# Optimization experiments

Hardware: AMD Instinct MI355X
Metric: run time of the kernel (lower is better)

## Reference

```python
import jax, jax.numpy as jnp
import numpy as np

B, N, C, H = 16, 1024, 768, 12
HD = C // H  # head_dim = 64


def setup_inputs() -> dict:
    key = jax.random.key(0)
    ks = jax.random.split(key, 3)
    scale = 1.0 / np.sqrt(C)
    x = jax.random.normal(ks[0], (B, N, C), dtype=jnp.float32)
    Wqkv = jax.random.normal(ks[1], (C, 3 * C), dtype=jnp.float32) * scale
    bqkv = jnp.zeros((3 * C,), dtype=jnp.float32)
    Wout = jax.random.normal(ks[2], (C, C), dtype=jnp.float32) * scale
    bout = jnp.zeros((C,), dtype=jnp.float32)
    return {"x": x, "Wqkv": Wqkv, "bqkv": bqkv, "Wout": Wout, "bout": bout}


def reference(x, Wqkv, bqkv, Wout, bout):
    # QKV projection: [B,N,3C] -> [B,N,3,H,HD]
    qkv = (x @ Wqkv + bqkv).reshape(B, N, 3, H, HD)
    q = qkv[:, :, 0].transpose(0, 2, 1, 3)  # [B,H,N,HD]
    k = qkv[:, :, 1].transpose(0, 2, 1, 3)
    v = qkv[:, :, 2].transpose(0, 2, 1, 3)
    # Patch attention (the only path that reaches the output: the source's
    # cross-image attention result is overwritten before out_proj, so it is
    # dead code). Dropout is identity in eval mode.
    scores = jnp.einsum("bhqd,bhkd->bhqk", q, k) / np.sqrt(HD).astype(np.float32)
    attn = jax.nn.softmax(scores, axis=-1)
    out = jnp.einsum("bhqk,bhkd->bhqd", attn, v)  # [B,H,N,HD]
    out = out.transpose(0, 2, 1, 3).reshape(B, N, C)
    return out @ Wout + bout
```

## Files before the change

kernel.cpp:

```cpp
#include <hip/hip_runtime.h>
#include <hip/hip_bf16.h>

#define B_   16
#define N_   1024
#define C_   768
#define H_   12
#define HD_  64
#define M_   16384
#define N1_  2304
#define NEG_BIG (-1e30f)
#define LOG2E 1.4426950408889634f

typedef __attribute__((ext_vector_type(8))) _Float16 f16x8;
typedef __attribute__((ext_vector_type(4))) float f32x4;
typedef __attribute__((ext_vector_type(16))) float f32x16;

__device__ __forceinline__ unsigned short f2h(float f) {
  _Float16 h = (_Float16)f;
  union { _Float16 h; unsigned short u; } c; c.h = h; return c.u;
}
__device__ __forceinline__ unsigned int cvtpk_f16(float a, float b) {
  unsigned int r;
  asm("v_cvt_pkrtz_f16_f32 %0, %1, %2" : "=v"(r) : "v"(a), "v"(b));
  return r;
}
__device__ __forceinline__ float exp2_asm(float x) {
  float r;
  asm("v_exp_f32 %0, %1" : "=v"(r) : "v"(x));
  return r;
}

__device__ __forceinline__ void gload_lds16(const void* g, void* l) {
  __builtin_amdgcn_global_load_lds(
      (const __attribute__((address_space(1))) void*)g,
      (__attribute__((address_space(3))) void*)l, 16, 0, 0);
}


typedef __attribute__((ext_vector_type(8))) short u16x8;

__global__ __launch_bounds__(256) void k_cvt_x(const float* __restrict__ x,
                                               unsigned short* __restrict__ xh) {
  long i = ((long)blockIdx.x * 256 + threadIdx.x) * 8;
  float4 a = *(const float4*)(x + i);
  float4 b = *(const float4*)(x + i + 4);
  u16x8 v;
  v[0] = (short)f2h(a.x); v[1] = (short)f2h(a.y);
  v[2] = (short)f2h(a.z); v[3] = (short)f2h(a.w);
  v[4] = (short)f2h(b.x); v[5] = (short)f2h(b.y);
  v[6] = (short)f2h(b.z); v[7] = (short)f2h(b.w);
  *(u16x8*)(xh + i) = v;
}

__global__ __launch_bounds__(256) void k_prep_wqkvT(const float* __restrict__ W,
                                                    unsigned short* __restrict__ Wt) {
  int tid = blockIdx.x * 256 + threadIdx.x;
  int n  = tid % N1_;
  int kc = tid / N1_;
  u16x8 v;
#pragma unroll
  for (int j = 0; j < 8; ++j)
    v[j] = (short)f2h(W[(long)(kc * 8 + j) * N1_ + n]);
  *(u16x8*)(Wt + (long)n * C_ + kc * 8) = v;
}

__global__ __launch_bounds__(256) void k_prep_wout(const float* __restrict__ W,
                                                   unsigned short* __restrict__ Wt) {
  int tid = blockIdx.x * 256 + threadIdx.x;
  int n  = tid % C_;
  int kc = tid / C_;
  u16x8 v;
#pragma unroll
  for (int j = 0; j < 8; ++j)
    v[j] = (short)f2h(W[(long)(kc * 8 + j) * C_ + n]);
  *(u16x8*)(Wt + (long)n * C_ + kc * 8) = v;
}

__global__ __launch_bounds__(256) void k_transposeV2(const unsigned short* __restrict__ qkvb,
                                                     unsigned short* __restrict__ Vt) {
  __shared__ unsigned char lt[16384];
  int wid = (blockIdx.x & 7) * 192 + (blockIdx.x >> 3);
  int bh = wid >> 3, nb = wid & 7;
  int b = bh / H_, h = bh % H_;
  long tok0 = (long)b * N_ + nb * 128;
  int t = threadIdx.x;
  int d0 = (t & 7) * 8;
#pragma unroll
  for (int it = 0; it < 4; ++it) {
    int nl = it * 32 + (t >> 3);
    u16x8 v = *(const u16x8*)(qkvb + (tok0 + nl) * N1_ + 1536 + h * HD_ + d0);
#pragma unroll
    for (int j = 0; j < 8; ++j) {
      int d = d0 + j;
      *(unsigned short*)(lt + d * 256 + ((nl * 2) ^ (((d >> 3) & 7) << 4))) =
          (unsigned short)v[j];
    }
  }
  __syncthreads();
  int l = t & 63, wv = t >> 6;
  int p = l & 1;
  int dbase = ((l >> 1) & 7) * 8 + (l >> 4) * 2;
#pragma unroll
  for (int rr = 0; rr < 4; ++rr) {
    int d = dbase + (rr & 1);
    int n0 = wv * 32 + (rr >> 1) * 16 + p * 8;
    u16x8 v = *(const u16x8*)(lt + d * 256 + ((n0 * 2) ^ (((d >> 3) & 7) << 4)));
    *(u16x8*)(Vt + ((long)bh * HD_ + d) * N_ + nb * 128 + n0) = v;
  }
}

template <int STAGE>
__global__ __launch_bounds__(512, 2)
void gemm256(const unsigned short* __restrict__ A,
             const unsigned short* __restrict__ Bt,
             const float* __restrict__ bias,
             void* __restrict__ out, int Kdim, int Ndim) {
  extern __shared__ unsigned char lds[];
  const int t = threadIdx.x;
  const int l = t & 63, w = t >> 6;
  const int g = l >> 4, lr = l & 15;
  const int wm = w >> 2, wn = w & 3;
  const int NB = Ndim >> 8;
  const int wgid = (blockIdx.x & 7) * (gridDim.x >> 3) + (blockIdx.x >> 3);
  const int mb = wgid / NB, nb = wgid % NB;
  const long m0 = (long)mb << 8, n0 = (long)nb << 8;
  const int T = Kdim >> 6;

  f32x4 acc[8][4];
  const f32x4 zz = {0.f, 0.f, 0.f, 0.f};
#pragma unroll
  for (int i = 0; i < 8; ++i)
#pragma unroll
    for (int j = 0; j < 4; ++j) acc[i][j] = zz;

  const long K2 = (long)Kdim * 2;
  const char* Ab = (const char*)A;
  const char* Bb = (const char*)Bt;
  const int sxcol = ((t & 7) * 16) ^ (((t >> 3) & 7) << 4);
  const int srowk = t >> 3;
  const int wvbase = w * 1024;

#define STAGE_A2(tile, i0)                                                   \
  {                                                                          \
    unsigned char* bufb_ = lds + ((tile) & 1) * 65536;                       \
    const char* As_ = Ab + (m0 + srowk) * K2 + (long)(tile) * 128 + sxcol;   \
    gload_lds16(As_ + (long)((i0) * 64) * K2,                                \
                (void*)(bufb_ + (i0) * 8192 + wvbase));                      \
    gload_lds16(As_ + (long)(((i0) + 1) * 64) * K2,                          \
                (void*)(bufb_ + ((i0) + 1) * 8192 + wvbase));                \
  }
#define STAGE_B2(tile, i0)                                                   \
  {                                                                          \
    unsigned char* bufb_ = lds + ((tile) & 1) * 65536 + 32768;               \
    const char* Bs_ = Bb + (n0 + srowk) * K2 + (long)(tile) * 128 + sxcol;   \
    gload_lds16(Bs_ + (long)((i0) * 64) * K2,                                \
                (void*)(bufb_ + (i0) * 8192 + wvbase));                      \
    gload_lds16(Bs_ + (long)(((i0) + 1) * 64) * K2,                          \
                (void*)(bufb_ + ((i0) + 1) * 8192 + wvbase));                \
  }

#define READ_A(ks, base)                                                     \
  _Pragma("unroll")                                                          \
  for (int mf = 0; mf < 8; ++mf) {                                           \
    int row = wm * 128 + mf * 16 + lr;                                       \
    af[mf] = *(const f16x8*)((base) + row * 128 +                            \
                             (((ks) * 64 + g * 16) ^ ((row & 7) << 4)));     \
  }
#define READ_B(ks, nh, base)                                                 \
  _Pragma("unroll")                                                          \
  for (int nf = 0; nf < 2; ++nf) {                                           \
    int row = wn * 64 + (nh) * 32 + nf * 16 + lr;                            \
    bfr[nf] = *(const f16x8*)((base) + 32768 + row * 128 +                   \
                              (((ks) * 64 + g * 16) ^ ((row & 7) << 4)));    \
  }
#define MFMA16(nh)                                                           \
  _Pragma("unroll")                                                          \
  for (int mf = 0; mf < 8; ++mf) {                                           \
    acc[mf][(nh) * 2 + 0] = __builtin_amdgcn_mfma_f32_16x16x32_f16(          \
        af[mf], bfr[0], acc[mf][(nh) * 2 + 0], 0, 0, 0);                     \
    acc[mf][(nh) * 2 + 1] = __builtin_amdgcn_mfma_f32_16x16x32_f16(          \
        af[mf], bfr[1], acc[mf][(nh) * 2 + 1], 0, 0, 0);                     \
  }
#define BAR()  __builtin_amdgcn_s_barrier(); asm volatile("" ::: "memory")

  STAGE_A2(0, 0); STAGE_A2(0, 2); STAGE_B2(0, 0); STAGE_B2(0, 2);
  STAGE_A2(1, 0); STAGE_A2(1, 2); STAGE_B2(1, 0); STAGE_B2(1, 2);
  asm volatile("s_waitcnt vmcnt(8)" ::: "memory");
  BAR();

  for (int tt = 0; tt < T; ++tt) {
    unsigned char* base = lds + (tt & 1) * 65536;
    f16x8 af[8], bfr[2];
    READ_A(0, base);
    READ_B(0, 0, base);
    if (tt >= 1 && tt + 1 < T) STAGE_B2(tt + 1, 0);
    BAR();
    __builtin_amdgcn_s_setprio(1);
    MFMA16(0);
    __builtin_amdgcn_s_setprio(0);
    BAR();
    READ_B(0, 1, base);
    if (tt >= 1 && tt + 1 < T) STAGE_B2(tt + 1, 2);
    BAR();
    __builtin_amdgcn_s_setprio(1);
    MFMA16(1);
    __builtin_amdgcn_s_setprio(0);
    BAR();
    READ_A(1, base);
    READ_B(1, 0, base);
    if (tt >= 1 && tt + 1 < T) STAGE_A2(tt + 1, 2);
    BAR();
    __builtin_amdgcn_s_setprio(1);
    MFMA16(0);
    __builtin_amdgcn_s_setprio(0);
    BAR();
    READ_B(1, 1, base);
    if (tt + 2 < T) STAGE_A2(tt + 2, 0);
    BAR();
    __builtin_amdgcn_s_setprio(1);
    MFMA16(1);
    __builtin_amdgcn_s_setprio(0);
    if (tt + 1 < T) {
      if (tt + 2 < T) { asm volatile("s_waitcnt vmcnt(2)" ::: "memory"); }
      else            { asm volatile("s_waitcnt vmcnt(0)" ::: "memory"); }
    }
    BAR();
  }
#undef STAGE_A2
#undef STAGE_B2
#undef READ_A
#undef READ_B
#undef MFMA16

  if (STAGE == 1) {
    float sc = (n0 < 768) ? 0.125f * LOG2E : 1.0f;
    unsigned short* cl = (unsigned short*)lds;
#pragma unroll
    for (int j = 0; j < 4; ++j) {
      int col = wn * 64 + (j >> 1) * 32 + (j & 1) * 16 + lr;
      float bv = bias[(int)n0 + col];
#pragma unroll
      for (int mf = 0; mf < 8; ++mf)
#pragma unroll
        for (int r = 0; r < 4; ++r) {
          int row = wm * 128 + mf * 16 + g * 4 + r;
          cl[row * 256 + col] = f2h((acc[mf][j][r] + bv) * sc);
        }
    }
    __syncthreads();
    unsigned short* o = (unsigned short*)out;
#pragma unroll
    for (int it = 0; it < 16; ++it) {
      int idx = it * 4096 + t * 8;
      int row = idx >> 8;
      int col = idx & 255;
      *(u16x8*)(o + (m0 + row) * N1_ + n0 + col) = *(const u16x8*)(cl + idx);
    }
  } else {
    float* o = (float*)out;
#pragma unroll
    for (int j = 0; j < 4; ++j) {
      int col = (int)n0 + wn * 64 + (j >> 1) * 32 + (j & 1) * 16 + lr;
      float bv = bias[col];
#pragma unroll
      for (int mf = 0; mf < 8; ++mf)
#pragma unroll
        for (int r = 0; r < 4; ++r) {
          long rowm = m0 + wm * 128 + mf * 16 + g * 4 + r;
          o[rowm * C_ + col] = acc[mf][j][r] + bv;
        }
    }
  }
#undef BAR
}

__global__ __launch_bounds__(256, 3)
void attn_fused(const unsigned short* __restrict__ qkvb,
                const unsigned short* __restrict__ Vt,
                unsigned short* __restrict__ Ofp) {
  __shared__ unsigned char lds[32768];
  const int t = threadIdx.x, l = t & 63, w = t >> 6;
  const int q32 = l & 31;
  const int hi = l >> 5;
  const int hi16 = hi * 16;
  const int wid = (blockIdx.x & 7) * 192 + (blockIdx.x >> 3);
  const int bh = wid >> 3, qb = wid & 7;
  const int b = bh / H_, h = bh % H_;
  const long tok0 = (long)b * N_;
  const int q0 = qb * 128 + w * 32;
  const long mytok = tok0 + q0 + q32;

  f16x8 qa[4];
#pragma unroll
  for (int cs = 0; cs < 4; ++cs)
    qa[cs] = *(const f16x8*)(qkvb + mytok * N1_ + h * HD_ + cs * 16 + hi * 8);

  const f32x16 zz16 = {0.f};
  f32x16 o0 = zz16, o1 = zz16;
  float mrun = NEG_BIG, lrun = 0.f;

  const int row0 = q32, row1 = 32 + q32;
  const int swz0 = (q32 & 7) << 4;

  const int sxs = ((t & 7) * 16) ^ (((t >> 3) & 7) << 4);
  const int wbase = (t & 192) * 16;
  const char* Vg = (const char*)(Vt + (long)bh * HD_ * N_);
  const char* Kg = (const char*)qkvb + ((tok0)*N1_ + C_ + h * HD_) * 2;

#define STAGE_KV(kv0, buf)                                                  \
  {                                                                         \
    _Pragma("unroll")                                                       \
    for (int i = 0; i < 2; ++i) {                                           \
      int row = i * 32 + (t >> 3);                                          \
      gload_lds16(Kg + ((long)(kv0 + row) * N1_) * 2 + sxs,                 \
                  (void*)((buf) + i * 4096 + wbase));                       \
    }                                                                       \
    _Pragma("unroll")                                                       \
    for (int i = 0; i < 2; ++i) {                                           \
      int row = i * 32 + (t >> 3);                                          \
      gload_lds16(Vg + ((long)row * N_ + (kv0)) * 2 + sxs,                  \
                  (void*)((buf) + 8192 + i * 4096 + wbase));                \
    }                                                                       \
  }

  STAGE_KV(0, lds);

#pragma unroll 2
  for (int tt = 0; tt < 16; ++tt) {
    unsigned char* curb = lds + (tt & 1) * 16384;
    unsigned char* nxtb = lds + ((tt & 1) ^ 1) * 16384;
    if (tt < 15) {
      STAGE_KV((tt + 1) * 64, nxtb);
      asm volatile("s_waitcnt vmcnt(4)" ::: "memory");
    } else {
      asm volatile("s_waitcnt vmcnt(0)" ::: "memory");
    }
    __builtin_amdgcn_s_barrier();
    __builtin_amdgcn_sched_barrier(0);

    f32x16 sa0 = zz16, sa1 = zz16;
#pragma unroll
    for (int cs = 0; cs < 4; ++cs) {
      f16x8 kf0 = *(const f16x8*)(curb + row0 * 128 + ((cs * 32 + hi16) ^ swz0));
      f16x8 kf1 = *(const f16x8*)(curb + row1 * 128 + ((cs * 32 + hi16) ^ swz0));
      sa0 = __builtin_amdgcn_mfma_f32_32x32x16_f16(kf0, qa[cs], sa0, 0, 0, 0);
      sa1 = __builtin_amdgcn_mfma_f32_32x32x16_f16(kf1, qa[cs], sa1, 0, 0, 0);
    }

    float tm[16];
#pragma unroll
    for (int i = 0; i < 16; ++i) tm[i] = fmaxf(sa0[i], sa1[i]);
#pragma unroll
    for (int s = 8; s >= 1; s >>= 1)
#pragma unroll
      for (int i = 0; i < s; ++i) tm[i] = fmaxf(tm[i], tm[i + s]);
    float mx = tm[0];
    mx = fmaxf(mx, __shfl_xor(mx, 32));
    if (!__all(mx <= mrun + 8.f)) {
      float mn = fmaxf(mrun, mx);
      float al = exp2_asm(mrun - mn);
      mrun = mn;
      lrun *= al;
      o0 *= al;
      o1 *= al;
    }
    float p0a[16], p1a[16];
#pragma unroll
    for (int i = 0; i < 16; ++i) p0a[i] = exp2_asm(sa0[i] - mrun);
#pragma unroll
    for (int i = 0; i < 16; ++i) p1a[i] = exp2_asm(sa1[i] - mrun);
    unsigned pk[2][4][2];
#pragma unroll
    for (int g = 0; g < 4; ++g) {
      pk[0][g][0] = cvtpk_f16(p0a[4 * g + 0], p0a[4 * g + 1]);
      pk[0][g][1] = cvtpk_f16(p0a[4 * g + 2], p0a[4 * g + 3]);
      pk[1][g][0] = cvtpk_f16(p1a[4 * g + 0], p1a[4 * g + 1]);
      pk[1][g][1] = cvtpk_f16(p1a[4 * g + 2], p1a[4 * g + 3]);
    }
    float ts[16];
#pragma unroll
    for (int i = 0; i < 16; ++i) ts[i] = p0a[i] + p1a[i];
#pragma unroll
    for (int s = 8; s >= 1; s >>= 1)
#pragma unroll
      for (int i = 0; i < s; ++i) ts[i] += ts[i + s];
    float rs = ts[0];
    rs += __shfl_xor(rs, 32);
    lrun += rs;

    f16x8 pb[4];
#pragma unroll
    for (int tk = 0; tk < 2; ++tk)
#pragma unroll
      for (int par = 0; par < 2; ++par) {
        unsigned a0 = pk[tk][2 * par][0], b0 = pk[tk][2 * par + 1][0];
        unsigned a1 = pk[tk][2 * par][1], b1 = pk[tk][2 * par + 1][1];
        asm("v_permlane32_swap_b32 %0, %1" : "+v"(a0), "+v"(b0));
        asm("v_permlane32_swap_b32 %0, %1" : "+v"(a1), "+v"(b1));
        union { unsigned u[4]; f16x8 v; } pw;
        pw.u[0] = a0; pw.u[1] = a1; pw.u[2] = b0; pw.u[3] = b1;
        pb[2 * tk + par] = pw.v;
      }

#pragma unroll
    for (int kb = 0; kb < 4; ++kb) {
      f16x8 vf0 = *(const f16x8*)(curb + 8192 + row0 * 128 + ((kb * 32 + hi16) ^ swz0));
      f16x8 vf1 = *(const f16x8*)(curb + 8192 + row1 * 128 + ((kb * 32 + hi16) ^ swz0));
      o0 = __builtin_amdgcn_mfma_f32_32x32x16_f16(vf0, pb[kb], o0, 0, 0, 0);
      o1 = __builtin_amdgcn_mfma_f32_32x32x16_f16(vf1, pb[kb], o1, 0, 0, 0);
    }
    __builtin_amdgcn_sched_barrier(0);
    asm volatile("s_waitcnt lgkmcnt(0)" ::: "memory");
    __builtin_amdgcn_s_barrier();
  }
#undef STAGE_KV

  float inv = 1.0f / lrun;
  unsigned short* obase = Ofp + mytok * C_ + h * HD_;
#pragma unroll
  for (int dt = 0; dt < 2; ++dt) {
#pragma unroll
    for (int rp = 0; rp < 8; ++rp) {
      int r = rp * 2;
      float v0 = (dt ? o1[r] : o0[r]) * inv;
      float v1 = (dt ? o1[r + 1] : o0[r + 1]) * inv;
      unsigned hw = cvtpk_f16(v0, v1);
      int d = dt * 32 + (r & 3) + 8 * (r >> 2) + 4 * hi;
      *(unsigned*)(obase + d) = hw;
    }
  }
}

extern "C" void kernel_launch(void* const* d_in, const int* in_sizes, int n_in,
                              void* d_out, int out_size, void* d_ws, size_t ws_size,
                              hipStream_t stream) {
  const float* x    = (const float*)d_in[0];
  const float* Wqkv = (const float*)d_in[1];
  const float* bqkv = (const float*)d_in[2];
  const float* Wout = (const float*)d_in[3];
  const float* bout = (const float*)d_in[4];

  char* ws = (char*)d_ws;
  unsigned short* qkvb  = (unsigned short*)(ws);
  unsigned short* Ofp   = (unsigned short*)(ws + 75497472L);
  unsigned short* xh    = (unsigned short*)(ws + 100663296L);
  unsigned short* Vt    = (unsigned short*)(ws + 100663296L);
  unsigned short* WqkvT = (unsigned short*)(ws + 125829120L);
  unsigned short* WoutT = (unsigned short*)(ws + 129368064L);

  hipFuncSetAttribute((const void*)gemm256<1>,
                      hipFuncAttributeMaxDynamicSharedMemorySize, 131072);
  hipFuncSetAttribute((const void*)gemm256<3>,
                      hipFuncAttributeMaxDynamicSharedMemorySize, 131072);

  k_cvt_x<<<6144, 256, 0, stream>>>(x, xh);
  k_prep_wqkvT<<<864, 256, 0, stream>>>(Wqkv, WqkvT);
  k_prep_wout<<<288, 256, 0, stream>>>(Wout, WoutT);
  gemm256<1><<<576, 512, 131072, stream>>>(xh, WqkvT, bqkv, (void*)qkvb, 768, 2304);
  k_transposeV2<<<1536, 256, 0, stream>>>(qkvb, Vt);
  attn_fused<<<1536, 256, 0, stream>>>(qkvb, Vt, Ofp);
  gemm256<3><<<192, 512, 131072, stream>>>(Ofp, WoutT, bout, d_out, 768, 768);
}
```

Baseline: 211.0 us.

## Replace 256-tile pipelined GEMM with simple 128-tile GEMM, retune attention max reduction

Swaps the 256x256 double-buffered, barrier-interleaved GEMM for a simpler 128x128 single-buffer GEMM with static 32KB LDS and more blocks, so more workgroups run concurrently per CU. The attention kernel's row-max reduction is restructured into three-input fmax chains and its occupancy hint rises from 3 to 4. The new GEMM loses the load/compute overlap and the higher per-tile reuse of the larger tiles, and it synchronises twice per K step.

```diff
diff --git a/kernel.cpp b/kernel.cpp
--- a/kernel.cpp
+++ b/kernel.cpp
@@ -110,171 +110,120 @@
 }
 
 template <int STAGE>
-__global__ __launch_bounds__(512, 2)
-void gemm256(const unsigned short* __restrict__ A,
+__global__ __launch_bounds__(256, 4)
+void gemm128(const unsigned short* __restrict__ A,
              const unsigned short* __restrict__ Bt,
              const float* __restrict__ bias,
              void* __restrict__ out, int Kdim, int Ndim) {
-  extern __shared__ unsigned char lds[];
+  __shared__ unsigned char lds[32768];
   const int t = threadIdx.x;
   const int l = t & 63, w = t >> 6;
   const int g = l >> 4, lr = l & 15;
-  const int wm = w >> 2, wn = w & 3;
-  const int NB = Ndim >> 8;
+  const int NB = Ndim >> 7;
   const int wgid = (blockIdx.x & 7) * (gridDim.x >> 3) + (blockIdx.x >> 3);
   const int mb = wgid / NB, nb = wgid % NB;
-  const long m0 = (long)mb << 8, n0 = (long)nb << 8;
-  const int T = Kdim >> 6;
-
-  f32x4 acc[8][4];
+  const long m0 = (long)mb << 7, n0 = (long)nb << 7;
+  const int wm = w >> 1, wn = w & 1;
+
+  f32x4 acc[4][4];
   const f32x4 zz = {0.f, 0.f, 0.f, 0.f};
 #pragma unroll
-  for (int i = 0; i < 8; ++i)
+  for (int i = 0; i < 4; ++i)
 #pragma unroll
     for (int j = 0; j < 4; ++j) acc[i][j] = zz;
 
-  const long K2 = (long)Kdim * 2;
+  int srow[4], sx[4];
+#pragma unroll
+  for (int i = 0; i < 4; ++i) {
+    int s = i * 4096 + t * 16;
+    int row = s >> 7;
+    srow[i] = row;
+    sx[i] = (s & 127) ^ ((row & 7) << 4);
+  }
   const char* Ab = (const char*)A;
   const char* Bb = (const char*)Bt;
-  const int sxcol = ((t & 7) * 16) ^ (((t >> 3) & 7) << 4);
-  const int srowk = t >> 3;
-  const int wvbase = w * 1024;
-
-#define STAGE_A2(tile, i0)                                                   \
-  {                                                                          \
-    unsigned char* bufb_ = lds + ((tile) & 1) * 65536;                       \
-    const char* As_ = Ab + (m0 + srowk) * K2 + (long)(tile) * 128 + sxcol;   \
-    gload_lds16(As_ + (long)((i0) * 64) * K2,                                \
-                (void*)(bufb_ + (i0) * 8192 + wvbase));                      \
-    gload_lds16(As_ + (long)(((i0) + 1) * 64) * K2,                          \
-                (void*)(bufb_ + ((i0) + 1) * 8192 + wvbase));                \
-  }
-#define STAGE_B2(tile, i0)                                                   \
-  {                                                                          \
-    unsigned char* bufb_ = lds + ((tile) & 1) * 65536 + 32768;               \
-    const char* Bs_ = Bb + (n0 + srowk) * K2 + (long)(tile) * 128 + sxcol;   \
-    gload_lds16(Bs_ + (long)((i0) * 64) * K2,                                \
-                (void*)(bufb_ + (i0) * 8192 + wvbase));                      \
-    gload_lds16(Bs_ + (long)(((i0) + 1) * 64) * K2,                          \
-                (void*)(bufb_ + ((i0) + 1) * 8192 + wvbase));                \
-  }
-
-#define READ_A(ks, base)                                                     \
-  _Pragma("unroll")                                                          \
-  for (int mf = 0; mf < 8; ++mf) {                                           \
-    int row = wm * 128 + mf * 16 + lr;                                       \
-    af[mf] = *(const f16x8*)((base) + row * 128 +                            \
-                             (((ks) * 64 + g * 16) ^ ((row & 7) << 4)));     \
-  }
-#define READ_B(ks, nh, base)                                                 \
-  _Pragma("unroll")                                                          \
-  for (int nf = 0; nf < 2; ++nf) {                                           \
-    int row = wn * 64 + (nh) * 32 + nf * 16 + lr;                            \
-    bfr[nf] = *(const f16x8*)((base) + 32768 + row * 128 +                   \
-                              (((ks) * 64 + g * 16) ^ ((row & 7) << 4)));    \
-  }
-#define MFMA16(nh)                                                           \
-  _Pragma("unroll")                                                          \
-  for (int mf = 0; mf < 8; ++mf) {                                           \
-    acc[mf][(nh) * 2 + 0] = __builtin_amdgcn_mfma_f32_16x16x32_f16(          \
-        af[mf], bfr[0], acc[mf][(nh) * 2 + 0], 0, 0, 0);                     \
-    acc[mf][(nh) * 2 + 1] = __builtin_amdgcn_mfma_f32_16x16x32_f16(          \
-        af[mf], bfr[1], acc[mf][(nh) * 2 + 1], 0, 0, 0);                     \
-  }
-#define BAR()  __builtin_amdgcn_s_barrier(); asm volatile("" ::: "memory")
-
-  STAGE_A2(0, 0); STAGE_A2(0, 2); STAGE_B2(0, 0); STAGE_B2(0, 2);
-  STAGE_A2(1, 0); STAGE_A2(1, 2); STAGE_B2(1, 0); STAGE_B2(1, 2);
-  asm volatile("s_waitcnt vmcnt(8)" ::: "memory");
-  BAR();
-
-  for (int tt = 0; tt < T; ++tt) {
-    unsigned char* base = lds + (tt & 1) * 65536;
-    f16x8 af[8], bfr[2];
-    READ_A(0, base);
-    READ_B(0, 0, base);
-    if (tt >= 1 && tt + 1 < T) STAGE_B2(tt + 1, 0);
-    BAR();
-    __builtin_amdgcn_s_setprio(1);
-    MFMA16(0);
-    __builtin_amdgcn_s_setprio(0);
-    BAR();
-    READ_B(0, 1, base);
-    if (tt >= 1 && tt + 1 < T) STAGE_B2(tt + 1, 2);
-    BAR();
-    __builtin_amdgcn_s_setprio(1);
-    MFMA16(1);
-    __builtin_amdgcn_s_setprio(0);
-    BAR();
-    READ_A(1, base);
-    READ_B(1, 0, base);
-    if (tt >= 1 && tt + 1 < T) STAGE_A2(tt + 1, 2);
-    BAR();
-    __builtin_amdgcn_s_setprio(1);
-    MFMA16(0);
-    __builtin_amdgcn_s_setprio(0);
-    BAR();
-    READ_B(1, 1, base);
-    if (tt + 2 < T) STAGE_A2(tt + 2, 0);
-    BAR();
-    __builtin_amdgcn_s_setprio(1);
-    MFMA16(1);
-    __builtin_amdgcn_s_setprio(0);
-    if (tt + 1 < T) {
-      if (tt + 2 < T) { asm volatile("s_waitcnt vmcnt(2)" ::: "memory"); }
-      else            { asm volatile("s_waitcnt vmcnt(0)" ::: "memory"); }
-    }
-    BAR();
-  }
-#undef STAGE_A2
-#undef STAGE_B2
-#undef READ_A
-#undef READ_B
-#undef MFMA16
+  const long K2 = (long)Kdim * 2;
+  const int wbase = (t & 192) * 16;
+
+  for (int kt = 0; kt < Kdim; kt += 64) {
+#pragma unroll
+    for (int i = 0; i < 4; ++i) {
+      const char* src = Ab + (m0 + srow[i]) * K2 + kt * 2 + sx[i];
+      gload_lds16(src, (void*)(lds + i * 4096 + wbase));
+    }
+#pragma unroll
+    for (int i = 0; i < 4; ++i) {
+      const char* src = Bb + (n0 + srow[i]) * K2 + kt * 2 + sx[i];
+      gload_lds16(src, (void*)(lds + 16384 + i * 4096 + wbase));
+    }
+    __syncthreads();
+#pragma unroll
+    for (int ks = 0; ks < 2; ++ks) {
+      f16x8 af[4], bfr[4];
+#pragma unroll
+      for (int mi = 0; mi < 4; ++mi) {
+        int row = wm * 64 + mi * 16 + lr;
+        int off = row * 128 + ((ks * 64 + g * 16) ^ ((row & 7) << 4));
+        af[mi] = *(const f16x8*)(lds + off);
+      }
+#pragma unroll
+      for (int ni = 0; ni < 4; ++ni) {
+        int row = wn * 64 + ni * 16 + lr;
+        int off = 16384 + row * 128 + ((ks * 64 + g * 16) ^ ((row & 7) << 4));
+        bfr[ni] = *(const f16x8*)(lds + off);
+      }
+#pragma unroll
+      for (int mi = 0; mi < 4; ++mi)
+#pragma unroll
+        for (int ni = 0; ni < 4; ++ni)
+          acc[mi][ni] = __builtin_amdgcn_mfma_f32_16x16x32_f16(
+              af[mi], bfr[ni], acc[mi][ni], 0, 0, 0);
+    }
+    __syncthreads();
+  }
 
   if (STAGE == 1) {
     float sc = (n0 < 768) ? 0.125f * LOG2E : 1.0f;
     unsigned short* cl = (unsigned short*)lds;
 #pragma unroll
-    for (int j = 0; j < 4; ++j) {
-      int col = wn * 64 + (j >> 1) * 32 + (j & 1) * 16 + lr;
+    for (int ni = 0; ni < 4; ++ni) {
+      int col = wn * 64 + ni * 16 + lr;
       float bv = bias[(int)n0 + col];
 #pragma unroll
-      for (int mf = 0; mf < 8; ++mf)
+      for (int mi = 0; mi < 4; ++mi)
 #pragma unroll
         for (int r = 0; r < 4; ++r) {
-          int row = wm * 128 + mf * 16 + g * 4 + r;
-          cl[row * 256 + col] = f2h((acc[mf][j][r] + bv) * sc);
+          int row = wm * 64 + mi * 16 + g * 4 + r;
+          cl[row * 128 + col] = f2h((acc[mi][ni][r] + bv) * sc);
         }
     }
     __syncthreads();
     unsigned short* o = (unsigned short*)out;
 #pragma unroll
-    for (int it = 0; it < 16; ++it) {
-      int idx = it * 4096 + t * 8;
-      int row = idx >> 8;
-      int col = idx & 255;
+    for (int it = 0; it < 8; ++it) {
+      int idx = it * 2048 + t * 8;
+      int row = idx >> 7;
+      int col = idx & 127;
       *(u16x8*)(o + (m0 + row) * N1_ + n0 + col) = *(const u16x8*)(cl + idx);
     }
   } else {
     float* o = (float*)out;
 #pragma unroll
-    for (int j = 0; j < 4; ++j) {
-      int col = (int)n0 + wn * 64 + (j >> 1) * 32 + (j & 1) * 16 + lr;
+    for (int ni = 0; ni < 4; ++ni) {
+      int col = (int)n0 + wn * 64 + ni * 16 + lr;
       float bv = bias[col];
 #pragma unroll
-      for (int mf = 0; mf < 8; ++mf)
+      for (int mi = 0; mi < 4; ++mi)
 #pragma unroll
         for (int r = 0; r < 4; ++r) {
-          long rowm = m0 + wm * 128 + mf * 16 + g * 4 + r;
-          o[rowm * C_ + col] = acc[mf][j][r] + bv;
+          long rowm = m0 + wm * 64 + mi * 16 + g * 4 + r;
+          o[rowm * C_ + col] = acc[mi][ni][r] + bv;
         }
     }
   }
-#undef BAR
-}
-
-__global__ __launch_bounds__(256, 3)
+}
+
+__global__ __launch_bounds__(256, 4)
 void attn_fused(const unsigned short* __restrict__ qkvb,
                 const unsigned short* __restrict__ Vt,
                 unsigned short* __restrict__ Ofp) {
@@ -347,14 +296,19 @@
       sa1 = __builtin_amdgcn_mfma_f32_32x32x16_f16(kf1, qa[cs], sa1, 0, 0, 0);
     }
 
-    float tm[16];
-#pragma unroll
-    for (int i = 0; i < 16; ++i) tm[i] = fmaxf(sa0[i], sa1[i]);
-#pragma unroll
-    for (int s = 8; s >= 1; s >>= 1)
-#pragma unroll
-      for (int i = 0; i < s; ++i) tm[i] = fmaxf(tm[i], tm[i + s]);
-    float mx = tm[0];
+    float tm[11];
+#pragma unroll
+    for (int i = 0; i < 5; ++i)
+      tm[i] = fmaxf(fmaxf(sa0[3 * i], sa0[3 * i + 1]), sa0[3 * i + 2]);
+    tm[5] = fmaxf(sa0[15], sa1[0]);
+#pragma unroll
+    for (int i = 0; i < 5; ++i)
+      tm[6 + i] = fmaxf(fmaxf(sa1[3 * i + 1], sa1[3 * i + 2]), sa1[3 * i + 3]);
+    float u0 = fmaxf(fmaxf(tm[0], tm[1]), tm[2]);
+    float u1 = fmaxf(fmaxf(tm[3], tm[4]), tm[5]);
+    float u2 = fmaxf(fmaxf(tm[6], tm[7]), tm[8]);
+    float u3 = fmaxf(fmaxf(tm[9], tm[10]), u0);
+    float mx = fmaxf(fmaxf(u1, u2), u3);
     mx = fmaxf(mx, __shfl_xor(mx, 32));
     if (!__all(mx <= mrun + 8.f)) {
       float mn = fmaxf(mrun, mx);
@@ -448,16 +402,11 @@
   unsigned short* WqkvT = (unsigned short*)(ws + 125829120L);
   unsigned short* WoutT = (unsigned short*)(ws + 129368064L);
 
-  hipFuncSetAttribute((const void*)gemm256<1>,
-                      hipFuncAttributeMaxDynamicSharedMemorySize, 131072);
-  hipFuncSetAttribute((const void*)gemm256<3>,
-                      hipFuncAttributeMaxDynamicSharedMemorySize, 131072);
-
   k_cvt_x<<<6144, 256, 0, stream>>>(x, xh);
   k_prep_wqkvT<<<864, 256, 0, stream>>>(Wqkv, WqkvT);
   k_prep_wout<<<288, 256, 0, stream>>>(Wout, WoutT);
-  gemm256<1><<<576, 512, 131072, stream>>>(xh, WqkvT, bqkv, (void*)qkvb, 768, 2304);
+  gemm128<1><<<2304, 256, 0, stream>>>(xh, WqkvT, bqkv, (void*)qkvb, 768, 2304);
   k_transposeV2<<<1536, 256, 0, stream>>>(qkvb, Vt);
   attn_fused<<<1536, 256, 0, stream>>>(qkvb, Vt, Ofp);
-  gemm256<3><<<192, 512, 131072, stream>>>(Ofp, WoutT, bout, d_out, 768, 768);
-}
+  gemm128<3><<<768, 256, 0, stream>>>(Ofp, WoutT, bout, d_out, 768, 768);
+}
```

New measurement: 188.8 us. 1.12x faster.
